# Kernel optimization log

Measured on AMD Instinct MI355X. Metric: run time of the kernel, lower is better.

Reference implementation:

```python
import jax, jax.numpy as jnp
import numpy as np


def setup_inputs() -> dict:
    key = jax.random.key(0)
    B, L, H, D = 8, 1024, 16, 64
    total_N = B * L
    qkv = jax.random.normal(key, (total_N, 3, H, D), dtype=jnp.float32)
    cu_seqlens = (jnp.arange(B + 1) * L).astype(jnp.int32)  # [B+1] cumulative lengths
    return {"qkv": qkv, "cu_seqlens": cu_seqlens, "max_seqlen": L}


def reference(qkv, cu_seqlens, max_seqlen):
    # qkv: [total_N, 3, H, D]; cu_seqlens: [B+1] int32
    total_N, _, H, D = qkv.shape
    scale = float(D) ** -0.5  # default softmax_scale = 1/sqrt(D)
    q, k, v = qkv[:, 0], qkv[:, 1], qkv[:, 2]  # each [total_N, H, D]

    starts = cu_seqlens[:-1]  # [B]
    ends = cu_seqlens[1:]     # [B]
    # Gather each ragged sequence into a padded [B, L, H, D] layout.
    pos = starts[:, None] + jnp.arange(max_seqlen, dtype=cu_seqlens.dtype)  # [B, L]
    valid = pos < ends[:, None]                                            # [B, L]
    idx = jnp.minimum(pos, total_N - 1)
    qp = q[idx]  # [B, L, H, D]
    kp = k[idx]
    vp = v[idx]

    # Per-sequence non-causal attention, softmax over keys of the same sequence.
    scores = jnp.einsum('bqhd,bkhd->bhqk', qp, kp) * scale  # [B, H, L, L]
    scores = jnp.where(valid[:, None, None, :], scores, jnp.float32(-1e30))
    attn = jax.nn.softmax(scores, axis=-1)
    outp = jnp.einsum('bhqk,bkhd->bqhd', attn, vp)  # [B, L, H, D]
    outp = outp * valid[:, :, None, None].astype(outp.dtype)  # zero padded queries

    # Scatter back to packed layout (invalid slots contribute zeros).
    out = jnp.zeros((total_N, H, D), dtype=qkv.dtype)
    out = out.at[idx.reshape(-1)].add(outp.reshape(-1, H, D))
    return out
```

## Files before the change

kernel.cpp:

```cpp
#include <hip/hip_runtime.h>


typedef __attribute__((ext_vector_type(4))) float f32x4;
typedef __attribute__((ext_vector_type(8))) __bf16 bf16x8;
typedef __attribute__((ext_vector_type(8))) unsigned short us8;

#if __has_builtin(__builtin_amdgcn_exp2f)
#define EXP2F __builtin_amdgcn_exp2f
#else
#define EXP2F exp2f
#endif
#if __has_builtin(__builtin_amdgcn_rcpf)
#define RCPF __builtin_amdgcn_rcpf
#else
#define RCPF(x) (1.0f / (x))
#endif

__device__ __forceinline__ unsigned pk_bf16(float a, float b) {
#if __has_builtin(__builtin_amdgcn_cvt_pk_bf16_f32)
  auto r = __builtin_amdgcn_cvt_pk_bf16_f32(a, b);
  return __builtin_bit_cast(unsigned, r);
#else
  unsigned ra = __builtin_bit_cast(unsigned, a) + 0x8000u;
  unsigned rb = __builtin_bit_cast(unsigned, b) + 0x8000u;
  return __builtin_amdgcn_perm(rb, ra, 0x07060302u);
#endif
}

#define LSTR 72
#define K_OFF 0
#define P_OFF (64 * LSTR)
#define VT_OFF (P_OFF + 256 * LSTR)
#define SMEM_USHORTS (VT_OFF + 80 * LSTR)

__launch_bounds__(512, 4)
__global__ void vla_fa_kernel(const float* __restrict__ qkv,
                              const int* __restrict__ cu,
                              float* __restrict__ out,
                              int B, int nflat) {
  __shared__ __align__(16) unsigned short smem[SMEM_USHORTS];
  const int tid = threadIdx.x;
  const int wave = tid >> 6, lane = tid & 63;
  const int lm = lane & 15, lq = lane >> 4;

  for (int i = tid; i < 16 * LSTR; i += 512) smem[VT_OFF + 64 * LSTR + i] = 0x3F80;

  const int BH = B * 16;
  for (int flat = blockIdx.x; flat < nflat; flat += gridDim.x) {
    const int b = flat % B;
    const int h = (flat / B) & 15;
    const int qb = flat / BH;
    const int s0 = cu[b], s1 = cu[b + 1];
    const int len = s1 - s0;
    if (qb * 256 >= len) continue;
    const int tmax = s1 - 1;

    __syncthreads();

    const float fs = 0.18033688011112042f;
#pragma unroll
    for (int p = 0; p < 8; ++p) {
      int idx = p * 512 + tid;
      int row = idx >> 4, c4 = idx & 15;
      int tok = s0 + qb * 256 + row;
      tok = tok > tmax ? tmax : tok;
      float4 v = *(const float4*)(qkv + (size_t)tok * 3072 + h * 64 + c4 * 4);
      uint2 w = {pk_bf16(v.x * fs, v.y * fs), pk_bf16(v.z * fs, v.w * fs)};
      *(uint2*)&smem[P_OFF + row * LSTR + c4 * 4] = w;
    }
    __syncthreads();

    bf16x8 qf[2][2];
#pragma unroll
    for (int rt = 0; rt < 2; ++rt)
#pragma unroll
      for (int ks = 0; ks < 2; ++ks)
        qf[rt][ks] = __builtin_bit_cast(
            bf16x8,
            *(const us8*)&smem[P_OFF + (wave * 32 + rt * 16 + lm) * LSTR + ks * 32 + lq * 8]);

    f32x4 Oacc[2][4];
    f32x4 lacc[2];
#pragma unroll
    for (int rt = 0; rt < 2; ++rt) {
      lacc[rt] = f32x4{0.f, 0.f, 0.f, 0.f};
#pragma unroll
      for (int dt = 0; dt < 4; ++dt) Oacc[rt][dt] = f32x4{0.f, 0.f, 0.f, 0.f};
    }

    const int krow = tid >> 3, kd8 = (tid & 7) * 8;

    const int nkt = (len + 63) >> 6;
    for (int kt = 0; kt < nkt; ++kt) {
      const int kbase = kt * 64;
      __syncthreads();

      int ktok = s0 + kbase + krow;
      ktok = ktok > tmax ? tmax : ktok;
      const float* kp = qkv + (size_t)ktok * 3072 + 1024 + h * 64 + kd8;
      float4 k0 = *(const float4*)kp;
      float4 k1 = *(const float4*)(kp + 4);

      float vv[2][4];
#pragma unroll
      for (int cc = 0; cc < 2; ++cc) {
        int c = wave * 2 + cc;
#pragma unroll
        for (int t = 0; t < 4; ++t) {
          int tok = s0 + kbase + c + t * 16;
          tok = tok > tmax ? tmax : tok;
          vv[cc][t] = qkv[(size_t)tok * 3072 + 2048 + h * 64 + lane];
        }
      }

      {
        uint4 kw = {pk_bf16(k0.x, k0.y), pk_bf16(k0.z, k0.w),
                    pk_bf16(k1.x, k1.y), pk_bf16(k1.z, k1.w)};
        *(uint4*)&smem[K_OFF + krow * LSTR + kd8] = kw;
      }
      __syncthreads();

      const bool partial = (len - kbase) < 64;
      f32x4 S[2][4];
#pragma unroll
      for (int rt = 0; rt < 2; ++rt)
#pragma unroll
        for (int nt = 0; nt < 4; ++nt) S[rt][nt] = f32x4{0.f, 0.f, 0.f, 0.f};
#pragma unroll
      for (int ks = 0; ks < 2; ++ks) {
        bf16x8 kfl[4];
#pragma unroll
        for (int nt = 0; nt < 4; ++nt)
          kfl[nt] = __builtin_bit_cast(
              bf16x8, *(const us8*)&smem[K_OFF + (nt * 16 + lm) * LSTR + ks * 32 + lq * 8]);
#pragma unroll
        for (int nt = 0; nt < 4; ++nt)
#pragma unroll
          for (int rt = 0; rt < 2; ++rt)
            S[rt][nt] =
                __builtin_amdgcn_mfma_f32_16x16x32_bf16(qf[rt][ks], kfl[nt], S[rt][nt], 0, 0, 0);
      }
#pragma unroll
      for (int rt = 0; rt < 2; ++rt) {
        if (partial) {
#pragma unroll
          for (int nt = 0; nt < 4; ++nt)
            if (kbase + nt * 16 + lm >= len)
              S[rt][nt] = f32x4{-1e30f, -1e30f, -1e30f, -1e30f};
        }
        int pbase = P_OFF + (wave * 32 + rt * 16 + lq * 4) * LSTR + lm * 4;
#pragma unroll
        for (int r = 0; r < 4; ++r) {
          uint2 w = {pk_bf16(EXP2F(S[rt][0][r]), EXP2F(S[rt][1][r])),
                     pk_bf16(EXP2F(S[rt][2][r]), EXP2F(S[rt][3][r]))};
          *(uint2*)&smem[pbase + r * LSTR] = w;
        }
      }

#pragma unroll
      for (int cc = 0; cc < 2; ++cc) {
        int c = wave * 2 + cc;
        uint2 w = {pk_bf16(vv[cc][0], vv[cc][1]), pk_bf16(vv[cc][2], vv[cc][3])};
        *(uint2*)&smem[VT_OFF + lane * LSTR + c * 4] = w;
      }
      __syncthreads();

#pragma unroll
      for (int ks = 0; ks < 2; ++ks) {
        bf16x8 vf[5];
#pragma unroll
        for (int dt = 0; dt < 5; ++dt)
          vf[dt] = __builtin_bit_cast(
              bf16x8, *(const us8*)&smem[VT_OFF + (dt * 16 + lm) * LSTR + ks * 32 + lq * 8]);
#pragma unroll
        for (int rt = 0; rt < 2; ++rt) {
          bf16x8 pf = __builtin_bit_cast(
              bf16x8,
              *(const us8*)&smem[P_OFF + (wave * 32 + rt * 16 + lm) * LSTR + ks * 32 + lq * 8]);
#pragma unroll
          for (int dt = 0; dt < 4; ++dt)
            Oacc[rt][dt] = __builtin_amdgcn_mfma_f32_16x16x32_bf16(pf, vf[dt], Oacc[rt][dt], 0, 0, 0);
          lacc[rt] = __builtin_amdgcn_mfma_f32_16x16x32_bf16(pf, vf[4], lacc[rt], 0, 0, 0);
        }
      }
    }

    const int rbase = qb * 256 + wave * 32;
#pragma unroll
    for (int rt = 0; rt < 2; ++rt) {
#pragma unroll
      for (int r = 0; r < 4; ++r) {
        int row = rbase + rt * 16 + lq * 4 + r;
        if (row < len) {
          float rl = RCPF(lacc[rt][r]);
          float* op = out + (size_t)(s0 + row) * 1024 + h * 64 + lm;
#pragma unroll
          for (int dt = 0; dt < 4; ++dt) op[dt * 16] = Oacc[rt][dt][r] * rl;
        }
      }
    }
  }
}

extern "C" void kernel_launch(void* const* d_in, const int* in_sizes, int n_in,
                              void* d_out, int out_size, void* d_ws, size_t ws_size,
                              hipStream_t stream) {
  const float* qkv = (const float*)d_in[0];
  const int* cu = (const int*)d_in[1];
  float* out = (float*)d_out;
  int B = in_sizes[1] - 1;
  int total_N = in_sizes[0] / (3 * 16 * 64);
  int qbmax = (total_N + 255) / 256;
  int nflat = B * 16 * qbmax;
  int nb = nflat < 512 ? nflat : 512;
  dim3 grid(nb), block(512, 1, 1);
  hipLaunchKernelGGL(vla_fa_kernel, grid, block, 0, stream, qkv, cu, out, B, nflat);
}
```

Baseline: 185.5 us.

## Switch to 32x32 MFMA with register-resident P, double-buffered K/V prefetch

Replaces the 16x16x32 MFMA tiling with 32x32x16 MFMA, computing S transposed so the exp'd probabilities stay in registers (via permlane32 swaps) instead of round-tripping through LDS. K/V tiles are double-buffered, with the global loads for the next tiles issued before the current tile's compute, which cuts the per-iteration barriers to one. Q is loaded directly into registers, and the row-sum is accumulated on the VALU rather than through an extra ones-column MFMA. This trades extra VGPR pressure and more complex lane shuffles for less LDS traffic and fewer synchronisations.

```diff
diff --git a/kernel.cpp b/kernel.cpp
--- a/kernel.cpp
+++ b/kernel.cpp
@@ -2,6 +2,7 @@
 
 
 typedef __attribute__((ext_vector_type(4))) float f32x4;
+typedef __attribute__((ext_vector_type(16))) float f32x16;
 typedef __attribute__((ext_vector_type(8))) __bf16 bf16x8;
 typedef __attribute__((ext_vector_type(8))) unsigned short us8;
 
@@ -27,25 +28,56 @@
 #endif
 }
 
-#define LSTR 72
-#define K_OFF 0
-#define P_OFF (64 * LSTR)
-#define VT_OFF (P_OFF + 256 * LSTR)
-#define SMEM_USHORTS (VT_OFF + 80 * LSTR)
+#define KSTR 72
+#define BUFUS (128 * KSTR)
+#define KO(b) ((b) * BUFUS)
+#define VO(b) ((b) * BUFUS + 64 * KSTR)
+
+#define BAR() asm volatile("s_waitcnt lgkmcnt(0)\n\ts_barrier" ::: "memory")
+
+#define ISSUE(KT)                                                             \
+  do {                                                                        \
+    const int kb_ = (KT) * 64;                                                \
+    int kt_ = s0 + kb_ + krow;                                                \
+    kt_ = kt_ > tmax ? tmax : kt_;                                            \
+    const float* kp_ = qkv + (size_t)kt_ * 3072 + 1024 + h64 + kd8;           \
+    k0 = *(const float4*)kp_;                                                 \
+    k1 = *(const float4*)(kp_ + 4);                                           \
+    _Pragma("unroll") for (int cc_ = 0; cc_ < 2; ++cc_) {                     \
+      _Pragma("unroll") for (int t_ = 0; t_ < 4; ++t_) {                      \
+        int vt_ = s0 + kb_ + vk0 + cc_ * 4 + t_;                              \
+        vt_ = vt_ > tmax ? tmax : vt_;                                        \
+        vv[cc_][t_] = qkv[(size_t)vt_ * 3072 + 2048 + h64 + lane];            \
+      }                                                                       \
+    }                                                                         \
+  } while (0)
+
+#define COMMIT(BI)                                                            \
+  do {                                                                        \
+    uint4 kw_ = {pk_bf16(k0.x, k0.y), pk_bf16(k0.z, k0.w),                    \
+                 pk_bf16(k1.x, k1.y), pk_bf16(k1.z, k1.w)};                   \
+    *(uint4*)&smem[KO(BI) + krow * KSTR + kd8] = kw_;                         \
+    _Pragma("unroll") for (int cc_ = 0; cc_ < 2; ++cc_) {                     \
+      uint2 vw_ = {pk_bf16(vv[cc_][0], vv[cc_][1]),                           \
+                   pk_bf16(vv[cc_][2], vv[cc_][3])};                          \
+      *(uint2*)&smem[VO(BI) + lane * KSTR + vk0 + cc_ * 4] = vw_;             \
+    }                                                                         \
+  } while (0)
 
 __launch_bounds__(512, 4)
 __global__ void vla_fa_kernel(const float* __restrict__ qkv,
                               const int* __restrict__ cu,
                               float* __restrict__ out,
                               int B, int nflat) {
-  __shared__ __align__(16) unsigned short smem[SMEM_USHORTS];
+  __shared__ __align__(16) unsigned short smem[2 * BUFUS];
+  __shared__ __align__(16) float ldsL[256];
   const int tid = threadIdx.x;
   const int wave = tid >> 6, lane = tid & 63;
-  const int lm = lane & 15, lq = lane >> 4;
-
-  for (int i = tid; i < 16 * LSTR; i += 512) smem[VT_OFF + 64 * LSTR + i] = 0x3F80;
-
+  const int q5 = lane & 31, hi = lane >> 5;
+  const int krow = tid >> 3, kd8 = (tid & 7) * 8;
+  const int vk0 = wave * 8;
   const int BH = B * 16;
+
   for (int flat = blockIdx.x; flat < nflat; flat += gridDim.x) {
     const int b = flat % B;
     const int h = (flat / B) & 15;
@@ -54,148 +86,121 @@
     const int len = s1 - s0;
     if (qb * 256 >= len) continue;
     const int tmax = s1 - 1;
-
-    __syncthreads();
+    const int h64 = h * 64;
+    const int nkt = (len + 63) >> 6;
+
+    float4 k0, k1;
+    float vv[2][4];
+    ISSUE(0);
 
     const float fs = 0.18033688011112042f;
-#pragma unroll
-    for (int p = 0; p < 8; ++p) {
-      int idx = p * 512 + tid;
-      int row = idx >> 4, c4 = idx & 15;
-      int tok = s0 + qb * 256 + row;
-      tok = tok > tmax ? tmax : tok;
-      float4 v = *(const float4*)(qkv + (size_t)tok * 3072 + h * 64 + c4 * 4);
-      uint2 w = {pk_bf16(v.x * fs, v.y * fs), pk_bf16(v.z * fs, v.w * fs)};
-      *(uint2*)&smem[P_OFF + row * LSTR + c4 * 4] = w;
+    int qtok = s0 + qb * 256 + wave * 32 + q5;
+    qtok = qtok > tmax ? tmax : qtok;
+    const float* qp = qkv + (size_t)qtok * 3072 + h64 + hi * 8;
+    bf16x8 qf[4];
+#pragma unroll
+    for (int ks = 0; ks < 4; ++ks) {
+      float4 a = *(const float4*)(qp + ks * 16);
+      float4 c = *(const float4*)(qp + ks * 16 + 4);
+      uint4 w = {pk_bf16(a.x * fs, a.y * fs), pk_bf16(a.z * fs, a.w * fs),
+                 pk_bf16(c.x * fs, c.y * fs), pk_bf16(c.z * fs, c.w * fs)};
+      qf[ks] = __builtin_bit_cast(bf16x8, w);
     }
-    __syncthreads();
-
-    bf16x8 qf[2][2];
-#pragma unroll
-    for (int rt = 0; rt < 2; ++rt)
-#pragma unroll
-      for (int ks = 0; ks < 2; ++ks)
-        qf[rt][ks] = __builtin_bit_cast(
-            bf16x8,
-            *(const us8*)&smem[P_OFF + (wave * 32 + rt * 16 + lm) * LSTR + ks * 32 + lq * 8]);
-
-    f32x4 Oacc[2][4];
-    f32x4 lacc[2];
-#pragma unroll
-    for (int rt = 0; rt < 2; ++rt) {
-      lacc[rt] = f32x4{0.f, 0.f, 0.f, 0.f};
-#pragma unroll
-      for (int dt = 0; dt < 4; ++dt) Oacc[rt][dt] = f32x4{0.f, 0.f, 0.f, 0.f};
+
+    f32x16 Oc[2];
+#pragma unroll
+    for (int dt = 0; dt < 2; ++dt)
+#pragma unroll
+      for (int i = 0; i < 16; ++i) Oc[dt][i] = 0.f;
+    float lacc[4] = {0.f, 0.f, 0.f, 0.f};
+
+    COMMIT(0);
+    if (nkt > 1) ISSUE(1);
+    BAR();
+
+    for (int kt = 0; kt < nkt; ++kt) {
+      const int cur = kt & 1;
+      const int kbase = kt * 64;
+      const bool partial = (len - kbase) < 64;
+      bf16x8 paf[4];
+
+#pragma unroll
+      for (int t = 0; t < 2; ++t) {
+        f32x16 S;
+#pragma unroll
+        for (int i = 0; i < 16; ++i) S[i] = 0.f;
+        const int krd = KO(cur) + (t * 32 + q5) * KSTR + hi * 8;
+        __builtin_amdgcn_s_setprio(1);
+#pragma unroll
+        for (int ks = 0; ks < 4; ++ks) {
+          bf16x8 kf =
+              __builtin_bit_cast(bf16x8, *(const us8*)&smem[krd + ks * 16]);
+          S = __builtin_amdgcn_mfma_f32_32x32x16_bf16(kf, qf[ks], S, 0, 0, 0);
+        }
+        __builtin_amdgcn_s_setprio(0);
+        if (partial) {
+#pragma unroll
+          for (int r = 0; r < 16; ++r) {
+            const int key = t * 32 + (r & 3) + ((r >> 2) << 3) + hi * 4;
+            if (kbase + key >= len) S[r] = -1e30f;
+          }
+        }
+        float p[16];
+#pragma unroll
+        for (int r = 0; r < 16; ++r) p[r] = EXP2F(S[r]);
+#pragma unroll
+        for (int r = 0; r < 16; ++r) lacc[r & 3] += p[r];
+#pragma unroll
+        for (int m = 0; m < 2; ++m) {
+          unsigned w0 = pk_bf16(p[m * 8 + 0], p[m * 8 + 1]);
+          unsigned w1 = pk_bf16(p[m * 8 + 2], p[m * 8 + 3]);
+          unsigned w2 = pk_bf16(p[m * 8 + 4], p[m * 8 + 5]);
+          unsigned w3 = pk_bf16(p[m * 8 + 6], p[m * 8 + 7]);
+          asm("v_permlane32_swap_b32 %0, %1" : "+v"(w0), "+v"(w2));
+          asm("v_permlane32_swap_b32 %0, %1" : "+v"(w1), "+v"(w3));
+          uint4 fw = {w0, w1, w2, w3};
+          paf[t * 2 + m] = __builtin_bit_cast(bf16x8, fw);
+        }
+      }
+
+      if (kt + 1 < nkt) {
+        COMMIT(cur ^ 1);
+        if (kt + 2 < nkt) ISSUE(kt + 2);
+      }
+
+      __builtin_amdgcn_s_setprio(1);
+#pragma unroll
+      for (int dt = 0; dt < 2; ++dt) {
+        const int vrd = VO(cur) + (dt * 32 + q5) * KSTR + hi * 8;
+#pragma unroll
+        for (int kc = 0; kc < 4; ++kc) {
+          bf16x8 vf =
+              __builtin_bit_cast(bf16x8, *(const us8*)&smem[vrd + kc * 16]);
+          Oc[dt] =
+              __builtin_amdgcn_mfma_f32_32x32x16_bf16(paf[kc], vf, Oc[dt], 0, 0, 0);
+        }
+      }
+      __builtin_amdgcn_s_setprio(0);
+      BAR();
     }
 
-    const int krow = tid >> 3, kd8 = (tid & 7) * 8;
-
-    const int nkt = (len + 63) >> 6;
-    for (int kt = 0; kt < nkt; ++kt) {
-      const int kbase = kt * 64;
-      __syncthreads();
-
-      int ktok = s0 + kbase + krow;
-      ktok = ktok > tmax ? tmax : ktok;
-      const float* kp = qkv + (size_t)ktok * 3072 + 1024 + h * 64 + kd8;
-      float4 k0 = *(const float4*)kp;
-      float4 k1 = *(const float4*)(kp + 4);
-
-      float vv[2][4];
-#pragma unroll
-      for (int cc = 0; cc < 2; ++cc) {
-        int c = wave * 2 + cc;
-#pragma unroll
-        for (int t = 0; t < 4; ++t) {
-          int tok = s0 + kbase + c + t * 16;
-          tok = tok > tmax ? tmax : tok;
-          vv[cc][t] = qkv[(size_t)tok * 3072 + 2048 + h * 64 + lane];
-        }
-      }
-
-      {
-        uint4 kw = {pk_bf16(k0.x, k0.y), pk_bf16(k0.z, k0.w),
-                    pk_bf16(k1.x, k1.y), pk_bf16(k1.z, k1.w)};
-        *(uint4*)&smem[K_OFF + krow * LSTR + kd8] = kw;
-      }
-      __syncthreads();
-
-      const bool partial = (len - kbase) < 64;
-      f32x4 S[2][4];
-#pragma unroll
-      for (int rt = 0; rt < 2; ++rt)
-#pragma unroll
-        for (int nt = 0; nt < 4; ++nt) S[rt][nt] = f32x4{0.f, 0.f, 0.f, 0.f};
-#pragma unroll
-      for (int ks = 0; ks < 2; ++ks) {
-        bf16x8 kfl[4];
-#pragma unroll
-        for (int nt = 0; nt < 4; ++nt)
-          kfl[nt] = __builtin_bit_cast(
-              bf16x8, *(const us8*)&smem[K_OFF + (nt * 16 + lm) * LSTR + ks * 32 + lq * 8]);
-#pragma unroll
-        for (int nt = 0; nt < 4; ++nt)
-#pragma unroll
-          for (int rt = 0; rt < 2; ++rt)
-            S[rt][nt] =
-                __builtin_amdgcn_mfma_f32_16x16x32_bf16(qf[rt][ks], kfl[nt], S[rt][nt], 0, 0, 0);
-      }
-#pragma unroll
-      for (int rt = 0; rt < 2; ++rt) {
-        if (partial) {
-#pragma unroll
-          for (int nt = 0; nt < 4; ++nt)
-            if (kbase + nt * 16 + lm >= len)
-              S[rt][nt] = f32x4{-1e30f, -1e30f, -1e30f, -1e30f};
-        }
-        int pbase = P_OFF + (wave * 32 + rt * 16 + lq * 4) * LSTR + lm * 4;
-#pragma unroll
-        for (int r = 0; r < 4; ++r) {
-          uint2 w = {pk_bf16(EXP2F(S[rt][0][r]), EXP2F(S[rt][1][r])),
-                     pk_bf16(EXP2F(S[rt][2][r]), EXP2F(S[rt][3][r]))};
-          *(uint2*)&smem[pbase + r * LSTR] = w;
-        }
-      }
-
-#pragma unroll
-      for (int cc = 0; cc < 2; ++cc) {
-        int c = wave * 2 + cc;
-        uint2 w = {pk_bf16(vv[cc][0], vv[cc][1]), pk_bf16(vv[cc][2], vv[cc][3])};
-        *(uint2*)&smem[VT_OFF + lane * LSTR + c * 4] = w;
-      }
-      __syncthreads();
-
-#pragma unroll
-      for (int ks = 0; ks < 2; ++ks) {
-        bf16x8 vf[5];
-#pragma unroll
-        for (int dt = 0; dt < 5; ++dt)
-          vf[dt] = __builtin_bit_cast(
-              bf16x8, *(const us8*)&smem[VT_OFF + (dt * 16 + lm) * LSTR + ks * 32 + lq * 8]);
-#pragma unroll
-        for (int rt = 0; rt < 2; ++rt) {
-          bf16x8 pf = __builtin_bit_cast(
-              bf16x8,
-              *(const us8*)&smem[P_OFF + (wave * 32 + rt * 16 + lm) * LSTR + ks * 32 + lq * 8]);
-#pragma unroll
-          for (int dt = 0; dt < 4; ++dt)
-            Oacc[rt][dt] = __builtin_amdgcn_mfma_f32_16x16x32_bf16(pf, vf[dt], Oacc[rt][dt], 0, 0, 0);
-          lacc[rt] = __builtin_amdgcn_mfma_f32_16x16x32_bf16(pf, vf[4], lacc[rt], 0, 0, 0);
-        }
-      }
-    }
-
+    float lt = (lacc[0] + lacc[1]) + (lacc[2] + lacc[3]);
+    lt += __shfl_xor(lt, 32, 64);
+    if (hi == 0) ldsL[wave * 32 + q5] = lt;
+    asm volatile("s_waitcnt lgkmcnt(0)" ::: "memory");
     const int rbase = qb * 256 + wave * 32;
 #pragma unroll
-    for (int rt = 0; rt < 2; ++rt) {
-#pragma unroll
-      for (int r = 0; r < 4; ++r) {
-        int row = rbase + rt * 16 + lq * 4 + r;
+    for (int g = 0; g < 4; ++g) {
+      f32x4 lv = *(const f32x4*)&ldsL[wave * 32 + g * 8 + hi * 4];
+#pragma unroll
+      for (int j = 0; j < 4; ++j) {
+        const int r = g * 4 + j;
+        const int row = rbase + g * 8 + hi * 4 + j;
         if (row < len) {
-          float rl = RCPF(lacc[rt][r]);
-          float* op = out + (size_t)(s0 + row) * 1024 + h * 64 + lm;
-#pragma unroll
-          for (int dt = 0; dt < 4; ++dt) op[dt * 16] = Oacc[rt][dt][r] * rl;
+          const float rl = RCPF(lv[j]);
+          float* op = out + (size_t)(s0 + row) * 1024 + h64 + q5;
+          op[0] = Oc[0][r] * rl;
+          op[32] = Oc[1][r] * rl;
         }
       }
     }
```

Result: slower. 198.6 us (+7.1%).
